# Kernel tuning notes

Hardware: AMD Instinct MI355X
Metric: run time of the kernel (lower is better)

Reference implementation:

```python
import jax, jax.numpy as jnp
import numpy as np
import math

DIM_IN = 768
RED = 256
FS = 384


def setup_inputs() -> dict:
    key = jax.random.key(0)
    ks = jax.random.split(key, 20)
    B, Nq, Nk = 16, 1024, FS
    inp = {
        "query_feature": jax.random.normal(ks[0], (B, Nq, DIM_IN), jnp.float32),
        "Input_feature": jax.random.normal(ks[1], (B, Nk, DIM_IN), jnp.float32),
    }
    # six q/k projections: Linear(dim_in -> reduce_dim), torch weight layout [out,in]
    names = ["q1", "q2", "q3", "k1", "k2", "k3"]
    for i, n in enumerate(names):
        inp[f"W{n}"] = 0.01 * jax.random.normal(ks[2 + i], (RED, DIM_IN), jnp.float32)
        inp[f"b{n}"] = jnp.zeros((RED,), jnp.float32)
    # self.layer: Linear(Fs_size -> 1)
    inp["layer_w"] = 0.01 * jax.random.normal(ks[10], (1, FS), jnp.float32)
    inp["layer_b"] = jnp.zeros((1,), jnp.float32)
    # output_layer: Linear(2*dim_in -> dim_in)
    inp["Wout"] = 0.01 * jax.random.normal(ks[11], (DIM_IN, 2 * DIM_IN), jnp.float32)
    inp["bout"] = jnp.zeros((DIM_IN,), jnp.float32)
    return inp


def _proj_center(x, W, b):
    # Linear then subtract per-feature mean over the token axis (dim=1)
    y = jnp.einsum("bnd,rd->bnr", x, W) + b
    return y - y.mean(axis=1, keepdims=True)


def reference(query_feature, Input_feature,
              Wq1, bq1, Wq2, bq2, Wq3, bq3,
              Wk1, bk1, Wk2, bk2, Wk3, bk3,
              layer_w, layer_b, Wout, bout):
    scale = 1.0 / math.sqrt(RED)
    q1 = _proj_center(query_feature, Wq1, bq1)
    q2 = _proj_center(query_feature, Wq2, bq2)
    q3 = _proj_center(query_feature, Wq3, bq3)
    k1 = _proj_center(Input_feature, Wk1, bk1)
    k2 = _proj_center(Input_feature, Wk2, bk2)
    k3 = _proj_center(Input_feature, Wk3, bk3)

    aw1 = jax.nn.softmax(jnp.einsum("bnr,bmr->bnm", q1, q2) * scale, axis=2)  # [B,Nq,Nq]
    aw2 = jax.nn.softmax(jnp.einsum("bnr,bmr->bnm", k1, k2) * scale, axis=2)  # [B,Nk,Nk]
    aw3 = jax.nn.softmax(jnp.einsum("bnr,bmr->bnm", q3, k3) * scale, axis=2)  # [B,Nq,Nk]

    attention_feature1 = jnp.einsum("bnm,bmd->bnd", aw1, query_feature)  # [B,Nq,D]
    hidden = jnp.einsum("bnm,om->bno", aw2, layer_w) + layer_b  # [B,Nk,1]
    hidden = jax.nn.softmax(hidden, axis=1)
    add = aw3 + jnp.swapaxes(hidden, 1, 2)  # broadcast [B,1,Nk]
    attention_feature2 = jnp.einsum("bnm,bmd->bnd", add, Input_feature)  # [B,Nq,D]

    cat = jnp.concatenate([attention_feature1, attention_feature2], axis=2)  # [B,Nq,2D]
    out = jnp.einsum("bnc,dc->bnd", cat, Wout) + bout
    return (cat, out)
```

## Files before the change

kernel.cpp:

```cpp
#include <hip/hip_runtime.h>

#define BATCH 16
#define NQ 1024
#define NK 384
#define DIM 768
#define RED 256
#define CATD 1536

typedef __attribute__((ext_vector_type(4))) float f32x4;
typedef __attribute__((ext_vector_type(8))) short short8;

__device__ __forceinline__ short f2bf(float f) {
    unsigned u = __builtin_bit_cast(unsigned, f);
    u = (u + 0x7FFF + ((u >> 16) & 1)) >> 16;
    return (short)u;
}

#define GLOAD_LDS16(g, l) __builtin_amdgcn_global_load_lds( \
    (const __attribute__((address_space(1))) unsigned int*)(g), \
    (__attribute__((address_space(3))) unsigned int*)(l), 16, 0, 0)

template<int MODE>
__global__ __launch_bounds__(256) void gemm_nt_mfma(
    const short* __restrict__ A, const short* __restrict__ B,
    float* __restrict__ Cf, short* __restrict__ Cb,
    const float* __restrict__ bias,
    int K, int lda, int ldb, int ldcf, int ldcb,
    long sA, long sB, long sCf, long sCb, float scale)
{
    __shared__ short Asl[128 * 64];
    __shared__ short Bsl[128 * 64];

    const unsigned nx = gridDim.x, ny = gridDim.y;
    unsigned lin = (blockIdx.z * ny + blockIdx.y) * nx + blockIdx.x;
    const unsigned nwg = nx * ny * gridDim.z;
    const unsigned qc = nwg >> 3, rc = nwg & 7;
    const unsigned xcd = lin & 7, pos = lin >> 3;
    unsigned nid = (xcd < rc ? xcd * (qc + 1) : rc * (qc + 1) + (xcd - rc) * qc) + pos;
    const unsigned bx = nid % nx;
    unsigned t = nid / nx;
    const unsigned by = t % ny;
    const unsigned bz = t / ny;

    const short* Ab = A + (long)bz * sA;
    const short* Bb = B + (long)bz * sB;
    const int m0 = by * 128, n0 = bx * 128;
    const int tid = threadIdx.x;
    const int lane = tid & 63, wid = tid >> 6;
    const int am0 = (wid >> 1) * 64, bn0 = (wid & 1) * 64;
    const int lr = lane & 15, lg = lane >> 4;

    f32x4 acc[4][4] = {};

    for (int k0 = 0; k0 < K; k0 += 64) {
        #pragma unroll
        for (int i = 0; i < 4; i++) {
            int e = (tid + i * 256) * 8;
            int r = e >> 6, c = e & 63;
            GLOAD_LDS16(Ab + (long)(m0 + r) * lda + k0 + c, Asl + e);
        }
        #pragma unroll
        for (int i = 0; i < 4; i++) {
            int e = (tid + i * 256) * 8;
            int r = e >> 6, c = e & 63;
            GLOAD_LDS16(Bb + (long)(n0 + r) * ldb + k0 + c, Bsl + e);
        }
        __syncthreads();
        #pragma unroll
        for (int ks = 0; ks < 2; ks++) {
            short8 af[4], bfv[4];
            #pragma unroll
            for (int m = 0; m < 4; m++)
                af[m] = *(const short8*)&Asl[(am0 + m * 16 + lr) * 64 + ks * 32 + lg * 8];
            #pragma unroll
            for (int n = 0; n < 4; n++)
                bfv[n] = *(const short8*)&Bsl[(bn0 + n * 16 + lr) * 64 + ks * 32 + lg * 8];
            #pragma unroll
            for (int m = 0; m < 4; m++)
                #pragma unroll
                for (int n = 0; n < 4; n++)
                    acc[m][n] = __builtin_amdgcn_mfma_f32_16x16x32_bf16(
                        af[m], bfv[n], acc[m][n], 0, 0, 0);
        }
        __syncthreads();
    }

    float* Cfb = (MODE != 1) ? Cf + (long)bz * sCf : nullptr;
    short* Cbb = (MODE == 1 || MODE == 2) ? Cb + (long)bz * sCb : nullptr;
    #pragma unroll
    for (int m = 0; m < 4; m++) {
        #pragma unroll
        for (int n = 0; n < 4; n++) {
            int col = n0 + bn0 + n * 16 + lr;
            #pragma unroll
            for (int j = 0; j < 4; j++) {
                long row = m0 + am0 + m * 16 + lg * 4 + j;
                float v = acc[m][n][j] * scale;
                if (MODE == 3) v += bias[col];
                if (MODE != 1) Cfb[row * ldcf + col] = v;
                if (MODE == 1 || MODE == 2) Cbb[row * ldcb + col] = f2bf(v);
            }
        }
    }
}

__global__ __launch_bounds__(256) void colsum(
    const float* __restrict__ X, float* __restrict__ mean, int N, int chunk)
{
    int b = blockIdx.x;
    int d = blockIdx.y * 256 + threadIdx.x;
    int n0 = blockIdx.z * chunk;
    float s = 0.f;
    for (int n = n0; n < n0 + chunk; n++)
        s += X[((long)b * N + n) * DIM + d];
    atomicAdd(&mean[b * DIM + d], s);
}

__global__ __launch_bounds__(256) void center_cvt(
    const float* __restrict__ X, const float* __restrict__ mean,
    short* __restrict__ Xc, int N, float invN)
{
    long i = (long)blockIdx.x * 256 + threadIdx.x;
    long tot8 = (long)BATCH * N * DIM / 8;
    if (i >= tot8) return;
    long e = i * 8;
    int d = (int)(e % DIM);
    int b = (int)(e / ((long)N * DIM));
    const float* mb = mean + b * DIM + d;
    const f32x4* s = (const f32x4*)(X + e);
    f32x4 x0 = s[0], x1 = s[1];
    short8 o;
    o[0] = f2bf(x0[0] - mb[0] * invN);
    o[1] = f2bf(x0[1] - mb[1] * invN);
    o[2] = f2bf(x0[2] - mb[2] * invN);
    o[3] = f2bf(x0[3] - mb[3] * invN);
    o[4] = f2bf(x1[0] - mb[4] * invN);
    o[5] = f2bf(x1[1] - mb[5] * invN);
    o[6] = f2bf(x1[2] - mb[6] * invN);
    o[7] = f2bf(x1[3] - mb[7] * invN);
    *(short8*)(Xc + e) = o;
}

struct WP { const float* p[7]; };
__global__ __launch_bounds__(256) void cvt_weights(
    WP wp, short* __restrict__ Wqb, short* __restrict__ Wkb,
    short* __restrict__ WoutB)
{
    const int WSZ = RED * DIM / 8;
    const int OSZ = DIM * CATD / 8;
    int i = blockIdx.x * 256 + threadIdx.x;
    if (i >= 6 * WSZ + OSZ) return;
    const float* src;
    short* dst;
    if (i < 6 * WSZ) {
        int w = i / WSZ, o = i - w * WSZ;
        src = wp.p[w] + (long)o * 8;
        dst = (w < 3 ? Wqb + (long)w * RED * DIM
                     : Wkb + (long)(w - 3) * RED * DIM) + (long)o * 8;
    } else {
        int o = i - 6 * WSZ;
        src = wp.p[6] + (long)o * 8;
        dst = WoutB + (long)o * 8;
    }
    const f32x4* s = (const f32x4*)src;
    f32x4 x0 = s[0], x1 = s[1];
    short8 o8;
    o8[0] = f2bf(x0[0]); o8[1] = f2bf(x0[1]); o8[2] = f2bf(x0[2]); o8[3] = f2bf(x0[3]);
    o8[4] = f2bf(x1[0]); o8[5] = f2bf(x1[1]); o8[6] = f2bf(x1[2]); o8[7] = f2bf(x1[3]);
    *(short8*)dst = o8;
}

__global__ __launch_bounds__(256) void transpose_cvt(
    const float* __restrict__ X, short* __restrict__ XT, int N)
{
    __shared__ short tile[32][33];
    int b = blockIdx.z;
    int n0 = blockIdx.x * 32, d0 = blockIdx.y * 32;
    int tx = threadIdx.x & 31, ty = threadIdx.x >> 5;
    const float* Xb = X + (long)b * N * DIM;
    #pragma unroll
    for (int i = 0; i < 4; i++) {
        int n = n0 + ty + i * 8;
        tile[ty + i * 8][tx] = f2bf(Xb[(long)n * DIM + d0 + tx]);
    }
    __syncthreads();
    short* XTb = XT + (long)b * DIM * N;
    #pragma unroll
    for (int i = 0; i < 4; i++) {
        int d = d0 + ty + i * 8;
        XTb[(long)d * N + n0 + tx] = tile[tx][ty + i * 8];
    }
}

template<int WRITE_P, int DOT>
__global__ __launch_bounds__(256) void softmax_rows(
    const float* __restrict__ S, short* __restrict__ P,
    const float* __restrict__ addv, const float* __restrict__ lw,
    float* __restrict__ dots, int L, int rows_per_batch)
{
    long row = blockIdx.x;
    const float* p = S + row * (long)L;
    const int tid = threadIdx.x;
    const int C = (L + 255) >> 8;
    float v[4];
    float mx = -3.0e38f;
    for (int c = 0; c < C; c++) {
        int i = tid + c * 256;
        v[c] = (i < L) ? p[i] : -3.0e38f;
        mx = fmaxf(mx, v[c]);
    }
    __shared__ float rmax[4], rsum[4], rdot[4];
    #pragma unroll
    for (int o = 1; o < 64; o <<= 1) mx = fmaxf(mx, __shfl_xor(mx, o));
    if ((tid & 63) == 0) rmax[tid >> 6] = mx;
    __syncthreads();
    mx = fmaxf(fmaxf(rmax[0], rmax[1]), fmaxf(rmax[2], rmax[3]));
    float s = 0.f, dt = 0.f;
    for (int c = 0; c < C; c++) {
        int i = tid + c * 256;
        float e = expf(v[c] - mx);
        v[c] = e;
        s += e;
        if (DOT) dt += (i < L) ? e * lw[i] : 0.f;
    }
    #pragma unroll
    for (int o = 1; o < 64; o <<= 1) s += __shfl_xor(s, o);
    if ((tid & 63) == 0) rsum[tid >> 6] = s;
    if (DOT) {
        #pragma unroll
        for (int o = 1; o < 64; o <<= 1) dt += __shfl_xor(dt, o);
        if ((tid & 63) == 0) rdot[tid >> 6] = dt;
    }
    __syncthreads();
    s = rsum[0] + rsum[1] + rsum[2] + rsum[3];
    float inv = 1.0f / s;
    if (DOT && tid == 0)
        dots[row] = (rdot[0] + rdot[1] + rdot[2] + rdot[3]) * inv;
    if (WRITE_P) {
        short* po = P + row * (long)L;
        if (addv) {
            int b = (int)(row / rows_per_batch);
            const float* av = addv + (long)b * L;
            for (int c = 0; c < C; c++) {
                int i = tid + c * 256;
                if (i < L) po[i] = f2bf(v[c] * inv + av[i]);
            }
        } else {
            for (int c = 0; c < C; c++) {
                int i = tid + c * 256;
                if (i < L) po[i] = f2bf(v[c] * inv);
            }
        }
    }
}

__global__ __launch_bounds__(384) void hid_softmax(
    const float* __restrict__ scores, float* __restrict__ hid)
{
    int b = blockIdx.x;
    int n = threadIdx.x;
    float s = scores[b * NK + n];
    __shared__ float red[6];
    float mx = s;
    #pragma unroll
    for (int o = 1; o < 64; o <<= 1) mx = fmaxf(mx, __shfl_xor(mx, o));
    int wid = n >> 6;
    if ((n & 63) == 0) red[wid] = mx;
    __syncthreads();
    mx = red[0];
    #pragma unroll
    for (int w = 1; w < 6; w++) mx = fmaxf(mx, red[w]);
    float e = expf(s - mx);
    float sm = e;
    #pragma unroll
    for (int o = 1; o < 64; o <<= 1) sm += __shfl_xor(sm, o);
    __syncthreads();
    if ((n & 63) == 0) red[wid] = sm;
    __syncthreads();
    sm = 0.f;
    #pragma unroll
    for (int w = 0; w < 6; w++) sm += red[w];
    hid[b * NK + n] = e / sm;
}

extern "C" void kernel_launch(void* const* d_in, const int* in_sizes, int n_in,
                              void* d_out, int out_size, void* d_ws, size_t ws_size,
                              hipStream_t stream)
{
    const float* Qf  = (const float*)d_in[0];
    const float* If  = (const float*)d_in[1];
    const float* lw  = (const float*)d_in[14];
    const float* bout= (const float*)d_in[17];

    float* cat = (float*)d_out;
    float* out = (float*)d_out + (long)BATCH * NQ * CATD;

    char* ws = (char*)d_ws;
    size_t off = 0;
    auto alloc = [&](size_t bytes) { char* p = ws + off; off += (bytes + 255) & ~(size_t)255; return p; };

    float* S     = (float*)alloc((size_t)BATCH * NQ * NQ * 4);
    short* Qc    = (short*)alloc((size_t)BATCH * NQ * DIM * 2);
    short* Kc    = (short*)alloc((size_t)BATCH * NK * DIM * 2);
    short* q_all = (short*)alloc((size_t)BATCH * NQ * 3 * RED * 2);
    short* k_all = (short*)alloc((size_t)BATCH * NK * 3 * RED * 2);
    short* P1    = (short*)alloc((size_t)BATCH * NQ * NQ * 2);
    short* P3    = (short*)alloc((size_t)BATCH * NQ * NK * 2);
    short* catbf = (short*)alloc((size_t)BATCH * NQ * CATD * 2);
    short* Wqb   = (short*)alloc((size_t)3 * RED * DIM * 2);
    short* Wkb   = (short*)alloc((size_t)3 * RED * DIM * 2);
    short* WoutB = (short*)alloc((size_t)DIM * CATD * 2);
    float* means = (float*)alloc((size_t)2 * BATCH * DIM * 4);
    float* scores= (float*)alloc((size_t)BATCH * NK * 4);
    float* hid   = (float*)alloc((size_t)BATCH * NK * 4);

    float* meanQ = means;
    float* meanK = means + BATCH * DIM;
    short* QfT = Qc;
    short* IfT = Kc;

    hipMemsetAsync(means, 0, (size_t)2 * BATCH * DIM * 4, stream);

    colsum<<<dim3(BATCH, DIM / 256, NQ / 128), 256, 0, stream>>>(Qf, meanQ, NQ, 128);
    colsum<<<dim3(BATCH, DIM / 256, NK / 128), 256, 0, stream>>>(If, meanK, NK, 128);
    center_cvt<<<(BATCH * NQ * DIM / 8 + 255) / 256, 256, 0, stream>>>(Qf, meanQ, Qc, NQ, 1.0f / NQ);
    center_cvt<<<(BATCH * NK * DIM / 8 + 255) / 256, 256, 0, stream>>>(If, meanK, Kc, NK, 1.0f / NK);

    {
        WP wp;
        wp.p[0] = (const float*)d_in[2];
        wp.p[1] = (const float*)d_in[4];
        wp.p[2] = (const float*)d_in[6];
        wp.p[3] = (const float*)d_in[8];
        wp.p[4] = (const float*)d_in[10];
        wp.p[5] = (const float*)d_in[12];
        wp.p[6] = (const float*)d_in[16];
        int total = 6 * (RED * DIM / 8) + DIM * CATD / 8;
        cvt_weights<<<(total + 255) / 256, 256, 0, stream>>>(wp, Wqb, Wkb, WoutB);
    }

    gemm_nt_mfma<1><<<dim3(6, BATCH * NQ / 128, 1), 256, 0, stream>>>(
        Qc, Wqb, nullptr, q_all, nullptr,
        DIM, DIM, DIM, 0, 3 * RED, 0, 0, 0, 0, 1.0f);
    gemm_nt_mfma<1><<<dim3(6, BATCH * NK / 128, 1), 256, 0, stream>>>(
        Kc, Wkb, nullptr, k_all, nullptr,
        DIM, DIM, DIM, 0, 3 * RED, 0, 0, 0, 0, 1.0f);

    transpose_cvt<<<dim3(NQ / 32, DIM / 32, BATCH), 256, 0, stream>>>(Qf, QfT, NQ);
    transpose_cvt<<<dim3(NK / 32, DIM / 32, BATCH), 256, 0, stream>>>(If, IfT, NK);

    const float scale = 0.0625f;
    const short* q1 = q_all;
    const short* q2 = q_all + RED;
    const short* q3 = q_all + 2 * RED;
    const short* k1 = k_all;
    const short* k2 = k_all + RED;
    const short* k3 = k_all + 2 * RED;
    const long sQ = (long)NQ * 3 * RED, sK = (long)NK * 3 * RED;

    gemm_nt_mfma<0><<<dim3(NQ / 128, NQ / 128, BATCH), 256, 0, stream>>>(
        q1, q2, S, nullptr, nullptr, RED, 3 * RED, 3 * RED, NQ, 0,
        sQ, sQ, (long)NQ * NQ, 0, scale);
    softmax_rows<1, 0><<<BATCH * NQ, 256, 0, stream>>>(S, P1, nullptr, nullptr, nullptr, NQ, NQ);

    gemm_nt_mfma<0><<<dim3(NK / 128, NK / 128, BATCH), 256, 0, stream>>>(
        k1, k2, S, nullptr, nullptr, RED, 3 * RED, 3 * RED, NK, 0,
        sK, sK, (long)NK * NK, 0, scale);
    softmax_rows<0, 1><<<BATCH * NK, 256, 0, stream>>>(S, nullptr, nullptr, lw, scores, NK, NK);
    hid_softmax<<<BATCH, NK, 0, stream>>>(scores, hid);

    gemm_nt_mfma<0><<<dim3(NK / 128, NQ / 128, BATCH), 256, 0, stream>>>(
        q3, k3, S, nullptr, nullptr, RED, 3 * RED, 3 * RED, NK, 0,
        sQ, sK, (long)NQ * NK, 0, scale);
    softmax_rows<1, 0><<<BATCH * NQ, 256, 0, stream>>>(S, P3, hid, nullptr, nullptr, NK, NQ);

    gemm_nt_mfma<2><<<dim3(DIM / 128, NQ / 128, BATCH), 256, 0, stream>>>(
        P1, QfT, cat, catbf, nullptr, NQ, NQ, NQ, CATD, CATD,
        (long)NQ * NQ, (long)DIM * NQ, (long)NQ * CATD, (long)NQ * CATD, 1.0f);
    gemm_nt_mfma<2><<<dim3(DIM / 128, NQ / 128, BATCH), 256, 0, stream>>>(
        P3, IfT, cat + DIM, catbf + DIM, nullptr, NK, NK, NK, CATD, CATD,
        (long)NQ * NK, (long)DIM * NK, (long)NQ * CATD, (long)NQ * CATD, 1.0f);

    gemm_nt_mfma<3><<<dim3(DIM / 128, NQ / 128, BATCH), 256, 0, stream>>>(
        catbf, WoutB, out, nullptr, bout, CATD, CATD, CATD, DIM, 0,
        (long)NQ * CATD, 0, (long)NQ * DIM, 0, 1.0f);
}
```

Measured before the change: 691.4 us.

## Batch independent GEMMs into routed launches, double-buffer LDS, fuse prep and softmax kernels

Replaces the templated GEMM with a descriptor-routed kernel that runs several independent GEMMs (Q/K projections, three score GEMMs, two attention-value GEMMs) in single launches. It double-buffers the LDS tiles so global-to-LDS loads overlap with MFMA compute. Centering and transpose conversion are fused into one prep kernel, and the two row softmaxes are merged into one launch using fast exp. Separate score buffers are allocated so the GEMMs can run together, which raises workspace use. LDS per block doubles, which may reduce occupancy.

```diff
diff --git a/kernel.cpp b/kernel.cpp
--- a/kernel.cpp
+++ b/kernel.cpp
@@ -20,61 +20,72 @@
     (const __attribute__((address_space(1))) unsigned int*)(g), \
     (__attribute__((address_space(3))) unsigned int*)(l), 16, 0, 0)
 
-template<int MODE>
-__global__ __launch_bounds__(256) void gemm_nt_mfma(
-    const short* __restrict__ A, const short* __restrict__ B,
-    float* __restrict__ Cf, short* __restrict__ Cb,
-    const float* __restrict__ bias,
-    int K, int lda, int ldb, int ldcf, int ldcb,
-    long sA, long sB, long sCf, long sCb, float scale)
-{
-    __shared__ short Asl[128 * 64];
-    __shared__ short Bsl[128 * 64];
-
-    const unsigned nx = gridDim.x, ny = gridDim.y;
-    unsigned lin = (blockIdx.z * ny + blockIdx.y) * nx + blockIdx.x;
-    const unsigned nwg = nx * ny * gridDim.z;
+struct GemmDesc {
+    const short* A; const short* B;
+    float* Cf; short* Cb; const float* bias;
+    int K, lda, ldb, ldcf, ldcb;
+    long sA, sB, sCf, sCb;
+    float scale;
+    int nx, ny;
+    int start;
+};
+
+__global__ __launch_bounds__(256) void gemm_routed(
+    GemmDesc d0, GemmDesc d1, GemmDesc d2, int nseg)
+{
+    __shared__ short Asl[2][128 * 64];
+    __shared__ short Bsl[2][128 * 64];
+
+    unsigned lin = blockIdx.x;
+    const unsigned nwg = gridDim.x;
     const unsigned qc = nwg >> 3, rc = nwg & 7;
     const unsigned xcd = lin & 7, pos = lin >> 3;
     unsigned nid = (xcd < rc ? xcd * (qc + 1) : rc * (qc + 1) + (xcd - rc) * qc) + pos;
-    const unsigned bx = nid % nx;
-    unsigned t = nid / nx;
-    const unsigned by = t % ny;
-    const unsigned bz = t / ny;
-
-    const short* Ab = A + (long)bz * sA;
-    const short* Bb = B + (long)bz * sB;
+
+    GemmDesc d = d0;
+    if (nseg > 1 && nid >= (unsigned)d1.start) d = d1;
+    if (nseg > 2 && nid >= (unsigned)d2.start) d = d2;
+
+    unsigned r = nid - (unsigned)d.start;
+    const unsigned bx = r % (unsigned)d.nx; r /= (unsigned)d.nx;
+    const unsigned by = r % (unsigned)d.ny;
+    const unsigned bz = r / (unsigned)d.ny;
+
+    const short* Ab = d.A + (long)bz * d.sA;
+    const short* Bb = d.B + (long)bz * d.sB;
     const int m0 = by * 128, n0 = bx * 128;
     const int tid = threadIdx.x;
     const int lane = tid & 63, wid = tid >> 6;
     const int am0 = (wid >> 1) * 64, bn0 = (wid & 1) * 64;
     const int lr = lane & 15, lg = lane >> 4;
+    const int lda = d.lda, ldb = d.ldb;
 
     f32x4 acc[4][4] = {};
 
-    for (int k0 = 0; k0 < K; k0 += 64) {
+    auto stage = [&](int buf, int k0) {
         #pragma unroll
         for (int i = 0; i < 4; i++) {
             int e = (tid + i * 256) * 8;
-            int r = e >> 6, c = e & 63;
-            GLOAD_LDS16(Ab + (long)(m0 + r) * lda + k0 + c, Asl + e);
+            int rr = e >> 6, c = e & 63;
+            GLOAD_LDS16(Ab + (long)(m0 + rr) * lda + k0 + c, &Asl[buf][e]);
         }
         #pragma unroll
         for (int i = 0; i < 4; i++) {
             int e = (tid + i * 256) * 8;
-            int r = e >> 6, c = e & 63;
-            GLOAD_LDS16(Bb + (long)(n0 + r) * ldb + k0 + c, Bsl + e);
+            int rr = e >> 6, c = e & 63;
+            GLOAD_LDS16(Bb + (long)(n0 + rr) * ldb + k0 + c, &Bsl[buf][e]);
         }
-        __syncthreads();
+    };
+    auto compute = [&](int buf) {
         #pragma unroll
         for (int ks = 0; ks < 2; ks++) {
             short8 af[4], bfv[4];
             #pragma unroll
             for (int m = 0; m < 4; m++)
-                af[m] = *(const short8*)&Asl[(am0 + m * 16 + lr) * 64 + ks * 32 + lg * 8];
+                af[m] = *(const short8*)&Asl[buf][(am0 + m * 16 + lr) * 64 + ks * 32 + lg * 8];
             #pragma unroll
             for (int n = 0; n < 4; n++)
-                bfv[n] = *(const short8*)&Bsl[(bn0 + n * 16 + lr) * 64 + ks * 32 + lg * 8];
+                bfv[n] = *(const short8*)&Bsl[buf][(bn0 + n * 16 + lr) * 64 + ks * 32 + lg * 8];
             #pragma unroll
             for (int m = 0; m < 4; m++)
                 #pragma unroll
@@ -82,25 +93,61 @@
                     acc[m][n] = __builtin_amdgcn_mfma_f32_16x16x32_bf16(
                         af[m], bfv[n], acc[m][n], 0, 0, 0);
         }
-        __syncthreads();
-    }
-
-    float* Cfb = (MODE != 1) ? Cf + (long)bz * sCf : nullptr;
-    short* Cbb = (MODE == 1 || MODE == 2) ? Cb + (long)bz * sCb : nullptr;
-    #pragma unroll
-    for (int m = 0; m < 4; m++) {
-        #pragma unroll
-        for (int n = 0; n < 4; n++) {
-            int col = n0 + bn0 + n * 16 + lr;
-            #pragma unroll
-            for (int j = 0; j < 4; j++) {
-                long row = m0 + am0 + m * 16 + lg * 4 + j;
-                float v = acc[m][n][j] * scale;
-                if (MODE == 3) v += bias[col];
-                if (MODE != 1) Cfb[row * ldcf + col] = v;
-                if (MODE == 1 || MODE == 2) Cbb[row * ldcb + col] = f2bf(v);
+    };
+
+    const int nt = d.K >> 6;
+    stage(0, 0);
+    __syncthreads();
+    int cur = 0;
+    for (int t = 0; t < nt; ++t) {
+        if (t + 1 < nt) stage(cur ^ 1, (t + 1) << 6);
+        compute(cur);
+        if (t + 1 < nt) { __syncthreads(); cur ^= 1; }
+    }
+
+    const float scale = d.scale;
+    float* Cfb = d.Cf ? d.Cf + (long)bz * d.sCf : nullptr;
+    short* Cbb = d.Cb ? d.Cb + (long)bz * d.sCb : nullptr;
+    if (Cfb && Cbb) {
+        #pragma unroll
+        for (int m = 0; m < 4; m++)
+            #pragma unroll
+            for (int n = 0; n < 4; n++) {
+                int col = n0 + bn0 + n * 16 + lr;
+                #pragma unroll
+                for (int j = 0; j < 4; j++) {
+                    long row = m0 + am0 + m * 16 + lg * 4 + j;
+                    float v = acc[m][n][j] * scale;
+                    Cfb[row * d.ldcf + col] = v;
+                    Cbb[row * d.ldcb + col] = f2bf(v);
+                }
             }
-        }
+    } else if (Cfb) {
+        const float* bias = d.bias;
+        #pragma unroll
+        for (int m = 0; m < 4; m++)
+            #pragma unroll
+            for (int n = 0; n < 4; n++) {
+                int col = n0 + bn0 + n * 16 + lr;
+                float bv = bias ? bias[col] : 0.f;
+                #pragma unroll
+                for (int j = 0; j < 4; j++) {
+                    long row = m0 + am0 + m * 16 + lg * 4 + j;
+                    Cfb[row * d.ldcf + col] = acc[m][n][j] * scale + bv;
+                }
+            }
+    } else {
+        #pragma unroll
+        for (int m = 0; m < 4; m++)
+            #pragma unroll
+            for (int n = 0; n < 4; n++) {
+                int col = n0 + bn0 + n * 16 + lr;
+                #pragma unroll
+                for (int j = 0; j < 4; j++) {
+                    long row = m0 + am0 + m * 16 + lg * 4 + j;
+                    Cbb[row * d.ldcb + col] = f2bf(acc[m][n][j] * scale);
+                }
+            }
     }
 }
 
@@ -108,37 +155,40 @@
     const float* __restrict__ X, float* __restrict__ mean, int N, int chunk)
 {
     int b = blockIdx.x;
-    int d = blockIdx.y * 256 + threadIdx.x;
+    int dd = blockIdx.y * 256 + threadIdx.x;
     int n0 = blockIdx.z * chunk;
     float s = 0.f;
     for (int n = n0; n < n0 + chunk; n++)
-        s += X[((long)b * N + n) * DIM + d];
-    atomicAdd(&mean[b * DIM + d], s);
-}
-
-__global__ __launch_bounds__(256) void center_cvt(
+        s += X[((long)b * N + n) * DIM + dd];
+    atomicAdd(&mean[b * DIM + dd], s);
+}
+
+template<int N>
+__global__ __launch_bounds__(256) void prep_input(
     const float* __restrict__ X, const float* __restrict__ mean,
-    short* __restrict__ Xc, int N, float invN)
-{
-    long i = (long)blockIdx.x * 256 + threadIdx.x;
-    long tot8 = (long)BATCH * N * DIM / 8;
-    if (i >= tot8) return;
-    long e = i * 8;
-    int d = (int)(e % DIM);
-    int b = (int)(e / ((long)N * DIM));
-    const float* mb = mean + b * DIM + d;
-    const f32x4* s = (const f32x4*)(X + e);
-    f32x4 x0 = s[0], x1 = s[1];
-    short8 o;
-    o[0] = f2bf(x0[0] - mb[0] * invN);
-    o[1] = f2bf(x0[1] - mb[1] * invN);
-    o[2] = f2bf(x0[2] - mb[2] * invN);
-    o[3] = f2bf(x0[3] - mb[3] * invN);
-    o[4] = f2bf(x1[0] - mb[4] * invN);
-    o[5] = f2bf(x1[1] - mb[5] * invN);
-    o[6] = f2bf(x1[2] - mb[6] * invN);
-    o[7] = f2bf(x1[3] - mb[7] * invN);
-    *(short8*)(Xc + e) = o;
+    short* __restrict__ Xc, short* __restrict__ XT, float invN)
+{
+    __shared__ short tile[32][33];
+    int b = blockIdx.z;
+    int n0 = blockIdx.x * 32, d0 = blockIdx.y * 32;
+    int tx = threadIdx.x & 31, ty = threadIdx.x >> 5;
+    const float* Xb = X + (long)b * N * DIM;
+    short* Xcb = Xc + (long)b * N * DIM;
+    float mv = mean[b * DIM + d0 + tx] * invN;
+    #pragma unroll
+    for (int i = 0; i < 4; i++) {
+        int n = n0 + ty + i * 8;
+        float x = Xb[(long)n * DIM + d0 + tx];
+        tile[ty + i * 8][tx] = f2bf(x);
+        Xcb[(long)n * DIM + d0 + tx] = f2bf(x - mv);
+    }
+    __syncthreads();
+    short* XTb = XT + (long)b * DIM * N;
+    #pragma unroll
+    for (int i = 0; i < 4; i++) {
+        int dd = d0 + ty + i * 8;
+        XTb[(long)dd * N + n0 + tx] = tile[tx][ty + i * 8];
+    }
 }
 
 struct WP { const float* p[7]; };
@@ -170,87 +220,108 @@
     *(short8*)dst = o8;
 }
 
-__global__ __launch_bounds__(256) void transpose_cvt(
-    const float* __restrict__ X, short* __restrict__ XT, int N)
-{
-    __shared__ short tile[32][33];
-    int b = blockIdx.z;
-    int n0 = blockIdx.x * 32, d0 = blockIdx.y * 32;
-    int tx = threadIdx.x & 31, ty = threadIdx.x >> 5;
-    const float* Xb = X + (long)b * N * DIM;
-    #pragma unroll
-    for (int i = 0; i < 4; i++) {
-        int n = n0 + ty + i * 8;
-        tile[ty + i * 8][tx] = f2bf(Xb[(long)n * DIM + d0 + tx]);
-    }
-    __syncthreads();
-    short* XTb = XT + (long)b * DIM * N;
-    #pragma unroll
-    for (int i = 0; i < 4; i++) {
-        int d = d0 + ty + i * 8;
-        XTb[(long)d * N + n0 + tx] = tile[tx][ty + i * 8];
-    }
-}
-
-template<int WRITE_P, int DOT>
-__global__ __launch_bounds__(256) void softmax_rows(
-    const float* __restrict__ S, short* __restrict__ P,
-    const float* __restrict__ addv, const float* __restrict__ lw,
-    float* __restrict__ dots, int L, int rows_per_batch)
-{
-    long row = blockIdx.x;
-    const float* p = S + row * (long)L;
+template<int L>
+__device__ __forceinline__ void softmax_body(
+    const float* __restrict__ p, short* __restrict__ po,
+    const float* __restrict__ addv)
+{
     const int tid = threadIdx.x;
     const int C = (L + 255) >> 8;
-    float v[4];
+    float v[C];
     float mx = -3.0e38f;
+    #pragma unroll
     for (int c = 0; c < C; c++) {
         int i = tid + c * 256;
         v[c] = (i < L) ? p[i] : -3.0e38f;
         mx = fmaxf(mx, v[c]);
     }
-    __shared__ float rmax[4], rsum[4], rdot[4];
+    __shared__ float rmax[4], rsum[4];
     #pragma unroll
     for (int o = 1; o < 64; o <<= 1) mx = fmaxf(mx, __shfl_xor(mx, o));
     if ((tid & 63) == 0) rmax[tid >> 6] = mx;
     __syncthreads();
     mx = fmaxf(fmaxf(rmax[0], rmax[1]), fmaxf(rmax[2], rmax[3]));
-    float s = 0.f, dt = 0.f;
+    float s = 0.f;
+    #pragma unroll
+    for (int c = 0; c < C; c++) {
+        float e = __expf(v[c] - mx);
+        v[c] = e;
+        s += e;
+    }
+    #pragma unroll
+    for (int o = 1; o < 64; o <<= 1) s += __shfl_xor(s, o);
+    if ((tid & 63) == 0) rsum[tid >> 6] = s;
+    __syncthreads();
+    s = rsum[0] + rsum[1] + rsum[2] + rsum[3];
+    float inv = 1.0f / s;
+    if (addv) {
+        #pragma unroll
+        for (int c = 0; c < C; c++) {
+            int i = tid + c * 256;
+            if (i < L) po[i] = f2bf(v[c] * inv + addv[i]);
+        }
+    } else {
+        #pragma unroll
+        for (int c = 0; c < C; c++) {
+            int i = tid + c * 256;
+            if (i < L) po[i] = f2bf(v[c] * inv);
+        }
+    }
+}
+
+__global__ __launch_bounds__(256) void softmax_two(
+    const float* __restrict__ S1, short* __restrict__ P1,
+    const float* __restrict__ S3, short* __restrict__ P3,
+    const float* __restrict__ hid)
+{
+    long row = blockIdx.x;
+    if (row < (long)BATCH * NQ) {
+        softmax_body<NQ>(S1 + row * NQ, P1 + row * NQ, nullptr);
+    } else {
+        row -= (long)BATCH * NQ;
+        int b = (int)(row / NQ);
+        softmax_body<NK>(S3 + row * NK, P3 + row * NK, hid + (long)b * NK);
+    }
+}
+
+__global__ __launch_bounds__(256) void softmax_dot(
+    const float* __restrict__ S2, const float* __restrict__ lw,
+    float* __restrict__ scores)
+{
+    long row = blockIdx.x;
+    const float* p = S2 + row * NK;
+    const int tid = threadIdx.x;
+    const int C = 2;
+    float v[C];
+    float mx = -3.0e38f;
+    #pragma unroll
     for (int c = 0; c < C; c++) {
         int i = tid + c * 256;
-        float e = expf(v[c] - mx);
-        v[c] = e;
+        v[c] = (i < NK) ? p[i] : -3.0e38f;
+        mx = fmaxf(mx, v[c]);
+    }
+    __shared__ float rmax[4], rsum[4], rdot[4];
+    #pragma unroll
+    for (int o = 1; o < 64; o <<= 1) mx = fmaxf(mx, __shfl_xor(mx, o));
+    if ((tid & 63) == 0) rmax[tid >> 6] = mx;
+    __syncthreads();
+    mx = fmaxf(fmaxf(rmax[0], rmax[1]), fmaxf(rmax[2], rmax[3]));
+    float s = 0.f, dt = 0.f;
+    #pragma unroll
+    for (int c = 0; c < C; c++) {
+        int i = tid + c * 256;
+        float e = __expf(v[c] - mx);
         s += e;
-        if (DOT) dt += (i < L) ? e * lw[i] : 0.f;
-    }
-    #pragma unroll
-    for (int o = 1; o < 64; o <<= 1) s += __shfl_xor(s, o);
-    if ((tid & 63) == 0) rsum[tid >> 6] = s;
-    if (DOT) {
-        #pragma unroll
-        for (int o = 1; o < 64; o <<= 1) dt += __shfl_xor(dt, o);
-        if ((tid & 63) == 0) rdot[tid >> 6] = dt;
-    }
-    __syncthreads();
-    s = rsum[0] + rsum[1] + rsum[2] + rsum[3];
-    float inv = 1.0f / s;
-    if (DOT && tid == 0)
-        dots[row] = (rdot[0] + rdot[1] + rdot[2] + rdot[3]) * inv;
-    if (WRITE_P) {
-        short* po = P + row * (long)L;
-        if (addv) {
-            int b = (int)(row / rows_per_batch);
-            const float* av = addv + (long)b * L;
-            for (int c = 0; c < C; c++) {
-                int i = tid + c * 256;
-                if (i < L) po[i] = f2bf(v[c] * inv + av[i]);
-            }
-        } else {
-            for (int c = 0; c < C; c++) {
-                int i = tid + c * 256;
-                if (i < L) po[i] = f2bf(v[c] * inv);
-            }
-        }
+        dt += (i < NK) ? e * lw[i] : 0.f;
+    }
+    #pragma unroll
+    for (int o = 1; o < 64; o <<= 1) { s += __shfl_xor(s, o); dt += __shfl_xor(dt, o); }
+    if ((tid & 63) == 0) { rsum[tid >> 6] = s; rdot[tid >> 6] = dt; }
+    __syncthreads();
+    if (tid == 0) {
+        s = rsum[0] + rsum[1] + rsum[2] + rsum[3];
+        dt = rdot[0] + rdot[1] + rdot[2] + rdot[3];
+        scores[row] = dt / s;
     }
 }
 
@@ -270,7 +341,7 @@
     mx = red[0];
     #pragma unroll
     for (int w = 1; w < 6; w++) mx = fmaxf(mx, red[w]);
-    float e = expf(s - mx);
+    float e = __expf(s - mx);
     float sm = e;
     #pragma unroll
     for (int o = 1; o < 64; o <<= 1) sm += __shfl_xor(sm, o);
@@ -299,9 +370,13 @@
     size_t off = 0;
     auto alloc = [&](size_t bytes) { char* p = ws + off; off += (bytes + 255) & ~(size_t)255; return p; };
 
-    float* S     = (float*)alloc((size_t)BATCH * NQ * NQ * 4);
+    float* S1    = (float*)alloc((size_t)BATCH * NQ * NQ * 4);
+    float* S2    = (float*)alloc((size_t)BATCH * NK * NK * 4);
+    float* S3    = (float*)alloc((size_t)BATCH * NQ * NK * 4);
     short* Qc    = (short*)alloc((size_t)BATCH * NQ * DIM * 2);
     short* Kc    = (short*)alloc((size_t)BATCH * NK * DIM * 2);
+    short* QfT   = (short*)alloc((size_t)BATCH * NQ * DIM * 2);
+    short* IfT   = (short*)alloc((size_t)BATCH * NK * DIM * 2);
     short* q_all = (short*)alloc((size_t)BATCH * NQ * 3 * RED * 2);
     short* k_all = (short*)alloc((size_t)BATCH * NK * 3 * RED * 2);
     short* P1    = (short*)alloc((size_t)BATCH * NQ * NQ * 2);
@@ -316,15 +391,14 @@
 
     float* meanQ = means;
     float* meanK = means + BATCH * DIM;
-    short* QfT = Qc;
-    short* IfT = Kc;
 
     hipMemsetAsync(means, 0, (size_t)2 * BATCH * DIM * 4, stream);
 
     colsum<<<dim3(BATCH, DIM / 256, NQ / 128), 256, 0, stream>>>(Qf, meanQ, NQ, 128);
     colsum<<<dim3(BATCH, DIM / 256, NK / 128), 256, 0, stream>>>(If, meanK, NK, 128);
-    center_cvt<<<(BATCH * NQ * DIM / 8 + 255) / 256, 256, 0, stream>>>(Qf, meanQ, Qc, NQ, 1.0f / NQ);
-    center_cvt<<<(BATCH * NK * DIM / 8 + 255) / 256, 256, 0, stream>>>(If, meanK, Kc, NK, 1.0f / NK);
+
+    prep_input<NQ><<<dim3(NQ / 32, DIM / 32, BATCH), 256, 0, stream>>>(Qf, meanQ, Qc, QfT, 1.0f / NQ);
+    prep_input<NK><<<dim3(NK / 32, DIM / 32, BATCH), 256, 0, stream>>>(If, meanK, Kc, IfT, 1.0f / NK);
 
     {
         WP wp;
@@ -339,49 +413,66 @@
         cvt_weights<<<(total + 255) / 256, 256, 0, stream>>>(wp, Wqb, Wkb, WoutB);
     }
 
-    gemm_nt_mfma<1><<<dim3(6, BATCH * NQ / 128, 1), 256, 0, stream>>>(
-        Qc, Wqb, nullptr, q_all, nullptr,
-        DIM, DIM, DIM, 0, 3 * RED, 0, 0, 0, 0, 1.0f);
-    gemm_nt_mfma<1><<<dim3(6, BATCH * NK / 128, 1), 256, 0, stream>>>(
-        Kc, Wkb, nullptr, k_all, nullptr,
-        DIM, DIM, DIM, 0, 3 * RED, 0, 0, 0, 0, 1.0f);
-
-    transpose_cvt<<<dim3(NQ / 32, DIM / 32, BATCH), 256, 0, stream>>>(Qf, QfT, NQ);
-    transpose_cvt<<<dim3(NK / 32, DIM / 32, BATCH), 256, 0, stream>>>(If, IfT, NK);
-
     const float scale = 0.0625f;
-    const short* q1 = q_all;
-    const short* q2 = q_all + RED;
-    const short* q3 = q_all + 2 * RED;
-    const short* k1 = k_all;
-    const short* k2 = k_all + RED;
-    const short* k3 = k_all + 2 * RED;
     const long sQ = (long)NQ * 3 * RED, sK = (long)NK * 3 * RED;
-
-    gemm_nt_mfma<0><<<dim3(NQ / 128, NQ / 128, BATCH), 256, 0, stream>>>(
-        q1, q2, S, nullptr, nullptr, RED, 3 * RED, 3 * RED, NQ, 0,
-        sQ, sQ, (long)NQ * NQ, 0, scale);
-    softmax_rows<1, 0><<<BATCH * NQ, 256, 0, stream>>>(S, P1, nullptr, nullptr, nullptr, NQ, NQ);
-
-    gemm_nt_mfma<0><<<dim3(NK / 128, NK / 128, BATCH), 256, 0, stream>>>(
-        k1, k2, S, nullptr, nullptr, RED, 3 * RED, 3 * RED, NK, 0,
-        sK, sK, (long)NK * NK, 0, scale);
-    softmax_rows<0, 1><<<BATCH * NK, 256, 0, stream>>>(S, nullptr, nullptr, lw, scores, NK, NK);
+    GemmDesc z = {};
+
+    {
+        GemmDesc dq = z, dk = z;
+        dq.A = Qc; dq.B = Wqb; dq.Cb = q_all;
+        dq.K = DIM; dq.lda = DIM; dq.ldb = DIM; dq.ldcb = 3 * RED;
+        dq.scale = 1.0f; dq.nx = 6; dq.ny = BATCH * NQ / 128; dq.start = 0;
+        dk = dq; dk.A = Kc; dk.B = Wkb; dk.Cb = k_all;
+        dk.ny = BATCH * NK / 128; dk.start = 6 * (BATCH * NQ / 128);
+        int total = dk.start + 6 * (BATCH * NK / 128);
+        gemm_routed<<<total, 256, 0, stream>>>(dq, dk, z, 2);
+    }
+
+    {
+        GemmDesc a = z, b = z, c = z;
+        a.A = q_all; a.B = q_all + RED; a.Cf = S1;
+        a.K = RED; a.lda = 3 * RED; a.ldb = 3 * RED; a.ldcf = NQ;
+        a.sA = sQ; a.sB = sQ; a.sCf = (long)NQ * NQ;
+        a.scale = scale; a.nx = NQ / 128; a.ny = NQ / 128; a.start = 0;
+        b.A = k_all; b.B = k_all + RED; b.Cf = S2;
+        b.K = RED; b.lda = 3 * RED; b.ldb = 3 * RED; b.ldcf = NK;
+        b.sA = sK; b.sB = sK; b.sCf = (long)NK * NK;
+        b.scale = scale; b.nx = NK / 128; b.ny = NK / 128;
+        b.start = a.nx * a.ny * BATCH;
+        c.A = q_all + 2 * RED; c.B = k_all + 2 * RED; c.Cf = S3;
+        c.K = RED; c.lda = 3 * RED; c.ldb = 3 * RED; c.ldcf = NK;
+        c.sA = sQ; c.sB = sK; c.sCf = (long)NQ * NK;
+        c.scale = scale; c.nx = NK / 128; c.ny = NQ / 128;
+        c.start = b.start + b.nx * b.ny * BATCH;
+        int total = c.start + c.nx * c.ny * BATCH;
+        gemm_routed<<<total, 256, 0, stream>>>(a, b, c, 3);
+    }
+
+    softmax_dot<<<BATCH * NK, 256, 0, stream>>>(S2, lw, scores);
     hid_softmax<<<BATCH, NK, 0, stream>>>(scores, hid);
-
-    gemm_nt_mfma<0><<<dim3(NK / 128, NQ / 128, BATCH), 256, 0, stream>>>(
-        q3, k3, S, nullptr, nullptr, RED, 3 * RED, 3 * RED, NK, 0,
-        sQ, sK, (long)NQ * NK, 0, scale);
-    softmax_rows<1, 0><<<BATCH * NQ, 256, 0, stream>>>(S, P3, hid, nullptr, nullptr, NK, NQ);
-
-    gemm_nt_mfma<2><<<dim3(DIM / 128, NQ / 128, BATCH), 256, 0, stream>>>(
-        P1, QfT, cat, catbf, nullptr, NQ, NQ, NQ, CATD, CATD,
-        (long)NQ * NQ, (long)DIM * NQ, (long)NQ * CATD, (long)NQ * CATD, 1.0f);
-    gemm_nt_mfma<2><<<dim3(DIM / 128, NQ / 128, BATCH), 256, 0, stream>>>(
-        P3, IfT, cat + DIM, catbf + DIM, nullptr, NK, NK, NK, CATD, CATD,
-        (long)NQ * NK, (long)DIM * NK, (long)NQ * CATD, (long)NQ * CATD, 1.0f);
-
-    gemm_nt_mfma<3><<<dim3(DIM / 128, NQ / 128, BATCH), 256, 0, stream>>>(
-        catbf, WoutB, out, nullptr, bout, CATD, CATD, CATD, DIM, 0,
-        (long)NQ * CATD, 0, (long)NQ * DIM, 0, 1.0f);
-}
+    softmax_two<<<2 * BATCH * NQ, 256, 0, stream>>>(S1, P1, S3, P3, hid);
+
+    {
+        GemmDesc p1 = z, p2 = z;
+        p1.A = P1; p1.B = QfT; p1.Cf = cat; p1.Cb = catbf;
+        p1.K = NQ; p1.lda = NQ; p1.ldb = NQ; p1.ldcf = CATD; p1.ldcb = CATD;
+        p1.sA = (long)NQ * NQ; p1.sB = (long)DIM * NQ;
+        p1.sCf = (long)NQ * CATD; p1.sCb = (long)NQ * CATD;
+        p1.scale = 1.0f; p1.nx = DIM / 128; p1.ny = NQ / 128; p1.start = 0;
+        p2 = p1;
+        p2.A = P3; p2.B = IfT; p2.Cf = cat + DIM; p2.Cb = catbf + DIM;
+        p2.K = NK; p2.lda = NK; p2.ldb = NK;
+        p2.sA = (long)NQ * NK; p2.sB = (long)DIM * NK;
+        p2.start = p1.nx * p1.ny * BATCH;
+        int total = 2 * p1.nx * p1.ny * BATCH;
+        gemm_routed<<<total, 256, 0, stream>>>(p1, p2, z, 2);
+    }
+
+    {
+        GemmDesc f = z;
+        f.A = catbf; f.B = WoutB; f.Cf = out; f.bias = bout;
+        f.K = CATD; f.lda = CATD; f.ldb = CATD; f.ldcf = DIM;
+        f.scale = 1.0f; f.nx = DIM / 128; f.ny = BATCH * NQ / 128; f.start = 0;
+        gemm_routed<<<f.nx * f.ny, 256, 0, stream>>>(f, z, z, 1);
+    }
+}
```

Result: faster. 666.7 us (-3.6%).
